# Kernel optimization log

Measured on AMD Instinct MI355X. Metric: run time of the kernel, lower is better.

## Reference

```python
import jax, jax.numpy as jnp
import numpy as np


def setup_inputs() -> dict:
    key = jax.random.key(0)
    k1, k2 = jax.random.split(key)
    B, C, H, W = 64, 64, 64, 64
    map1 = jax.random.normal(k1, (B, C, H, W), dtype=jnp.float32)
    map2 = jax.random.normal(k2, (B, C, H, W), dtype=jnp.float32)
    return {"map1": map1, "map2": map2}


def reference(map1, map2):
    # conv2d(map1, map2) with equal spatial dims -> [B,B,1,1]; .diag() keeps
    # only the per-sample full cross-correlation: c_i = sum(map1[i]*map2[i]).
    corr = jnp.einsum('bchw,bchw->b', map1, map2)          # [B]
    corr = corr / jnp.linalg.norm(corr)                    # L2-normalize over batch
    corr = 1.0 - corr
    # out[i] = map1[i] + map2[i] * corr[i]
    return map1 + map2 * corr[:, None, None, None]
```

## Files before the change

### kernel.cpp

```cpp
#include <hip/hip_runtime.h>


#define THREADS 256
#define NBATCH 64
#define RBPB 16
#define ABPB 64
#define V4B 65536
#define RV4BLK 4096
#define AV4BLK 1024

__global__ __launch_bounds__(THREADS, 4) void corr_reduce_kernel(
    const float4* __restrict__ m1, const float4* __restrict__ m2,
    float* __restrict__ partials) {
  const int b = blockIdx.y;
  const int base = b * V4B + blockIdx.x * RV4BLK + threadIdx.x;

  float acc0 = 0.f, acc1 = 0.f, acc2 = 0.f, acc3 = 0.f;
#pragma unroll
  for (int r = 0; r < 4; ++r) {
    float4 a[4], v[4];
    const int o = base + r * 4 * THREADS;
#pragma unroll
    for (int k = 0; k < 4; ++k) a[k] = m1[o + k * THREADS];
#pragma unroll
    for (int k = 0; k < 4; ++k) v[k] = m2[o + k * THREADS];
#pragma unroll
    for (int k = 0; k < 4; ++k) {
      acc0 = fmaf(a[k].x, v[k].x, acc0);
      acc1 = fmaf(a[k].y, v[k].y, acc1);
      acc2 = fmaf(a[k].z, v[k].z, acc2);
      acc3 = fmaf(a[k].w, v[k].w, acc3);
    }
  }
  float acc = (acc0 + acc1) + (acc2 + acc3);

#pragma unroll
  for (int off = 32; off > 0; off >>= 1) acc += __shfl_xor(acc, off);

  __shared__ float wsum[4];
  if ((threadIdx.x & 63) == 0) wsum[threadIdx.x >> 6] = acc;
  __syncthreads();
  if (threadIdx.x == 0)
    partials[b * RBPB + blockIdx.x] = (wsum[0] + wsum[1]) + (wsum[2] + wsum[3]);
}

__global__ __launch_bounds__(THREADS, 4) void corr_apply_kernel(
    const float4* __restrict__ m1, const float4* __restrict__ m2,
    const float4* __restrict__ partials4, float4* __restrict__ out) {
  const int b = blockIdx.y;
  const int base = b * V4B + blockIdx.x * AV4BLK + threadIdx.x;

  float4 a[4], v[4];
#pragma unroll
  for (int k = 0; k < 4; ++k) a[k] = m1[base + k * THREADS];
#pragma unroll
  for (int k = 0; k < 4; ++k) v[k] = m2[base + k * THREADS];

  const float4 p = partials4[threadIdx.x];
  __builtin_amdgcn_sched_barrier(0);

  float s = (p.x + p.y) + (p.z + p.w);
  s += __shfl_xor(s, 1);
  s += __shfl_xor(s, 2);

  __shared__ float csh[NBATCH];
  __shared__ float c_sh;
  if ((threadIdx.x & 3) == 0) csh[threadIdx.x >> 2] = s;
  __syncthreads();
  if (threadIdx.x < 64) {
    float cv = csh[threadIdx.x];
    float sq = cv * cv;
#pragma unroll
    for (int off = 32; off > 0; off >>= 1) sq += __shfl_xor(sq, off);
    if (threadIdx.x == 0) c_sh = 1.0f - csh[b] * rsqrtf(sq);
  }
  __syncthreads();
  const float c = c_sh;

#pragma unroll
  for (int k = 0; k < 4; ++k) {
    float4 o;
    o.x = fmaf(v[k].x, c, a[k].x);
    o.y = fmaf(v[k].y, c, a[k].y);
    o.z = fmaf(v[k].z, c, a[k].z);
    o.w = fmaf(v[k].w, c, a[k].w);
    out[base + k * THREADS] = o;
  }
}

extern "C" void kernel_launch(void* const* d_in, const int* in_sizes, int n_in,
                              void* d_out, int out_size, void* d_ws, size_t ws_size,
                              hipStream_t stream) {
  const float4* m1 = (const float4*)d_in[0];
  const float4* m2 = (const float4*)d_in[1];
  float* partials = (float*)d_ws;
  float4* out = (float4*)d_out;

  dim3 rgrid(RBPB, NBATCH);
  dim3 agrid(ABPB, NBATCH);
  corr_reduce_kernel<<<rgrid, THREADS, 0, stream>>>(m1, m2, partials);
  corr_apply_kernel<<<agrid, THREADS, 0, stream>>>(m1, m2, (const float4*)partials, out);
}
```

Measured before the change: 187.5 us.

## Fuse reduce and apply into cooperative kernel caching map2 in LDS and registers

```diff
diff --git a/kernel.cpp b/kernel.cpp
--- a/kernel.cpp
+++ b/kernel.cpp
@@ -1,29 +1,109 @@
 #include <hip/hip_runtime.h>
+#include <hip/hip_cooperative_groups.h>
+
+namespace cg = cooperative_groups;
 
 
 #define THREADS 256
 #define NBATCH 64
-#define RBPB 16
+#define BPB 16
+#define V4B 65536
+#define V4SEG 4096
+#define K_LDS 8
+#define K_REG 8
 #define ABPB 64
-#define V4B 65536
-#define RV4BLK 4096
 #define AV4BLK 1024
+
+__global__ __launch_bounds__(THREADS, 4) void corr_fused_kernel(
+    const float4* __restrict__ m1, const float4* __restrict__ m2,
+    float* __restrict__ partials, float4* __restrict__ out) {
+  __shared__ float4 v_lds[K_LDS * THREADS];
+  __shared__ float wsum[4];
+
+  const int t = threadIdx.x;
+  const int b = blockIdx.y;
+  const int base = b * V4B + blockIdx.x * V4SEG + t;
+
+  float4 vreg[K_REG];
+  float acc0 = 0.f, acc1 = 0.f, acc2 = 0.f, acc3 = 0.f;
+#pragma unroll
+  for (int r = 0; r < 4; ++r) {
+    float4 a[4], v[4];
+#pragma unroll
+    for (int k = 0; k < 4; ++k) a[k] = m1[base + (4 * r + k) * THREADS];
+#pragma unroll
+    for (int k = 0; k < 4; ++k) v[k] = m2[base + (4 * r + k) * THREADS];
+#pragma unroll
+    for (int k = 0; k < 4; ++k) {
+      const int kk = 4 * r + k;
+      acc0 = fmaf(a[k].x, v[k].x, acc0);
+      acc1 = fmaf(a[k].y, v[k].y, acc1);
+      acc2 = fmaf(a[k].z, v[k].z, acc2);
+      acc3 = fmaf(a[k].w, v[k].w, acc3);
+      if (kk < K_LDS) v_lds[kk * THREADS + t] = v[k];
+      else            vreg[kk - K_LDS] = v[k];
+    }
+  }
+  float acc = (acc0 + acc1) + (acc2 + acc3);
+#pragma unroll
+  for (int off = 32; off > 0; off >>= 1) acc += __shfl_xor(acc, off);
+  if ((t & 63) == 0) wsum[t >> 6] = acc;
+  __syncthreads();
+  if (t == 0)
+    partials[b * BPB + blockIdx.x] = (wsum[0] + wsum[1]) + (wsum[2] + wsum[3]);
+  __threadfence();
+
+  cg::this_grid().sync();
+
+  const int lane = t & 63;
+  const float4* p4 = (const float4*)partials;
+  float s = 0.f;
+#pragma unroll
+  for (int j = 0; j < 4; ++j) {
+    const float4 p = p4[4 * lane + j];
+    s += (p.x + p.y) + (p.z + p.w);
+  }
+  float sq = s * s;
+#pragma unroll
+  for (int off = 32; off > 0; off >>= 1) sq += __shfl_xor(sq, off);
+  const float cb = __shfl(s, b);
+  const float c = 1.0f - cb * rsqrtf(sq);
+
+#pragma unroll
+  for (int r = 0; r < 4; ++r) {
+    float4 a[4];
+#pragma unroll
+    for (int k = 0; k < 4; ++k) a[k] = m1[base + (4 * r + k) * THREADS];
+#pragma unroll
+    for (int k = 0; k < 4; ++k) {
+      const int kk = 4 * r + k;
+      const float4 v = (kk < K_LDS) ? v_lds[kk * THREADS + t]
+                                    : vreg[kk - K_LDS];
+      float4 o;
+      o.x = fmaf(v.x, c, a[k].x);
+      o.y = fmaf(v.y, c, a[k].y);
+      o.z = fmaf(v.z, c, a[k].z);
+      o.w = fmaf(v.w, c, a[k].w);
+      out[base + (4 * r + k) * THREADS] = o;
+    }
+  }
+}
+
 
 __global__ __launch_bounds__(THREADS, 4) void corr_reduce_kernel(
     const float4* __restrict__ m1, const float4* __restrict__ m2,
     float* __restrict__ partials) {
   const int b = blockIdx.y;
-  const int base = b * V4B + blockIdx.x * RV4BLK + threadIdx.x;
+  const int base = b * V4B + blockIdx.x * V4SEG + threadIdx.x;
 
   float acc0 = 0.f, acc1 = 0.f, acc2 = 0.f, acc3 = 0.f;
 #pragma unroll
   for (int r = 0; r < 4; ++r) {
     float4 a[4], v[4];
-    const int o = base + r * 4 * THREADS;
 #pragma unroll
-    for (int k = 0; k < 4; ++k) a[k] = m1[o + k * THREADS];
+    for (int k = 0; k < 4; ++k) a[k] = m1[base + (4 * r + k) * THREADS];
 #pragma unroll
-    for (int k = 0; k < 4; ++k) v[k] = m2[o + k * THREADS];
+    for (int k = 0; k < 4; ++k) v[k] = m2[base + (4 * r + k) * THREADS];
 #pragma unroll
     for (int k = 0; k < 4; ++k) {
       acc0 = fmaf(a[k].x, v[k].x, acc0);
@@ -33,15 +113,13 @@
     }
   }
   float acc = (acc0 + acc1) + (acc2 + acc3);
-
 #pragma unroll
   for (int off = 32; off > 0; off >>= 1) acc += __shfl_xor(acc, off);
-
   __shared__ float wsum[4];
   if ((threadIdx.x & 63) == 0) wsum[threadIdx.x >> 6] = acc;
   __syncthreads();
   if (threadIdx.x == 0)
-    partials[b * RBPB + blockIdx.x] = (wsum[0] + wsum[1]) + (wsum[2] + wsum[3]);
+    partials[b * BPB + blockIdx.x] = (wsum[0] + wsum[1]) + (wsum[2] + wsum[3]);
 }
 
 __global__ __launch_bounds__(THREADS, 4) void corr_apply_kernel(
@@ -96,8 +174,26 @@
   float* partials = (float*)d_ws;
   float4* out = (float4*)d_out;
 
-  dim3 rgrid(RBPB, NBATCH);
-  dim3 agrid(ABPB, NBATCH);
-  corr_reduce_kernel<<<rgrid, THREADS, 0, stream>>>(m1, m2, partials);
-  corr_apply_kernel<<<agrid, THREADS, 0, stream>>>(m1, m2, (const float4*)partials, out);
+  dim3 grid(BPB, NBATCH);
+
+  hipError_t err = hipErrorUnknown;
+  int occ = 0, ncu = 0, dev = 0;
+  if (hipGetDevice(&dev) == hipSuccess &&
+      hipDeviceGetAttribute(&ncu, hipDeviceAttributeMultiprocessorCount,
+                            dev) == hipSuccess &&
+      hipOccupancyMaxActiveBlocksPerMultiprocessor(
+          &occ, corr_fused_kernel, THREADS, 0) == hipSuccess &&
+      occ * ncu >= BPB * NBATCH) {
+    void* args[] = {(void*)&m1, (void*)&m2, (void*)&partials, (void*)&out};
+    err = hipLaunchCooperativeKernel(corr_fused_kernel, grid, dim3(THREADS),
+                                     args, 0, stream);
+  }
+
+  if (err != hipSuccess) {
+    (void)hipGetLastError();
+    dim3 agrid(ABPB, NBATCH);
+    corr_reduce_kernel<<<grid, THREADS, 0, stream>>>(m1, m2, partials);
+    corr_apply_kernel<<<agrid, THREADS, 0, stream>>>(
+        m1, m2, (const float4*)partials, out);
+  }
 }
```

After: 189.1 us. No clear change (+0.8%).
